# Kernel tuning notes

Measured on AMD Instinct MI355X. Metric: run time of the kernel, lower is better.

The kernel has to match this reference:

```python
import jax, jax.numpy as jnp
import numpy as np


def setup_inputs() -> dict:
    key = jax.random.key(0)
    ks = jax.random.split(key, 9)
    B, S, E, H, D = 8, 1000, 1024, 16, 64
    sc = 0.02
    return {
        "x": jax.random.normal(ks[0], (B, S, E), dtype=jnp.float32),
        "wq": jax.random.normal(ks[1], (H, E, D), dtype=jnp.float32) * sc,
        "bq": jax.random.normal(ks[2], (H, D), dtype=jnp.float32) * sc,
        "wk": jax.random.normal(ks[3], (H, E, D), dtype=jnp.float32) * sc,
        "bk": jax.random.normal(ks[4], (H, D), dtype=jnp.float32) * sc,
        "wv": jax.random.normal(ks[5], (H, E, D), dtype=jnp.float32) * sc,
        "bv": jax.random.normal(ks[6], (H, D), dtype=jnp.float32) * sc,
        "wp": jax.random.normal(ks[7], (E, E), dtype=jnp.float32) * sc,
        "bp": jax.random.normal(ks[8], (E,), dtype=jnp.float32) * sc,
    }


def reference(x, wq, bq, wk, bk, wv, bv, wp, bp):
    B, S, E = x.shape
    H, _, D = wq.shape
    # per-head projections, all heads batched: [B,H,S,D]
    q = jnp.einsum('bse,hed->bhsd', x, wq) + bq[None, :, None, :]
    k = jnp.einsum('bse,hed->bhsd', x, wk) + bk[None, :, None, :]
    v = jnp.einsum('bse,hed->bhsd', x, wv) + bv[None, :, None, :]
    # NOTE: original scales by sqrt(seq_len), not sqrt(head_dim)
    scores = jnp.einsum('bhsd,bhtd->bhst', q, k) / jnp.asarray(S, x.dtype) ** 0.5
    causal = jnp.tril(jnp.ones((S, S), dtype=bool))  # mask[:S,:S] == 1 keeps
    scores = jnp.where(causal, scores, jnp.asarray(-jnp.inf, x.dtype))
    attn = jax.nn.softmax(scores, axis=-1)
    z = jnp.einsum('bhst,bhtd->bhsd', attn, v)
    # concat heads in head order -> [B,S,E]
    y = z.transpose(0, 2, 1, 3).reshape(B, S, E)
    # projection then exact GELU (dropout is identity at eval)
    return jax.nn.gelu(jnp.einsum('bse,ef->bsf', y, wp) + bp, approximate=False)
```

## Files before the change

### kernel.cpp

```cpp
#include <hip/hip_runtime.h>
#include <hip/hip_bf16.h>
#include <math.h>

constexpr int B_ = 8, S_ = 1000, E_ = 1024, H_ = 16, D_ = 64;
constexpr int M_ = B_ * S_;

using bf16x8 = __attribute__((ext_vector_type(8))) __bf16;
using u16x8  = __attribute__((ext_vector_type(8))) unsigned short;
using f32x4  = __attribute__((ext_vector_type(4))) float;

static __device__ __forceinline__ unsigned short f2bf(float f) {
    union { float f; unsigned u; } c; c.f = f;
    return (unsigned short)((c.u + 0x7FFF + ((c.u >> 16) & 1)) >> 16);
}
static __device__ __forceinline__ unsigned short f2bf_fast(float f) {
    union { float f; unsigned u; } c; c.f = f;
    return (unsigned short)((c.u + 0x8000) >> 16);
}
static __device__ __forceinline__ float bfr2f(unsigned short s) {
    union { unsigned u; float f; } c; c.u = ((unsigned)s) << 16;
    return c.f;
}

__global__ __launch_bounds__(256) void cast_x_kernel(
    const float* __restrict__ x, unsigned short* __restrict__ xbf)
{
    const size_t i = ((size_t)blockIdx.x * 256 + threadIdx.x) * 4;
    float4 v = *(const float4*)(x + i);
    ushort4 o;
    o.x = f2bf(v.x); o.y = f2bf(v.y); o.z = f2bf(v.z); o.w = f2bf(v.w);
    *(ushort4*)(xbf + i) = o;
}

__global__ __launch_bounds__(256) void transpose_wqkv_kernel(
    const float* __restrict__ wq, const float* __restrict__ wk,
    const float* __restrict__ wv, unsigned short* __restrict__ WT)
{
    __shared__ unsigned short Ts[64 * 65];
    const int et = blockIdx.x, zh = blockIdx.y;
    const int z = zh >> 4, h = zh & 15;
    const float* src = (z == 0 ? wq : z == 1 ? wk : wv) + (size_t)h * E_ * D_;

    const int d = threadIdx.x & 63;
    const int e0 = threadIdx.x >> 6;
    #pragma unroll
    for (int p = 0; p < 16; ++p) {
        const int e = e0 + p * 4;
        Ts[d * 65 + e] = f2bf(src[(size_t)(et * 64 + e) * D_ + d]);
    }
    __syncthreads();
    const int e = threadIdx.x & 63;
    const int d0 = threadIdx.x >> 6;
    #pragma unroll
    for (int p = 0; p < 16; ++p) {
        const int dd = d0 + p * 4;
        WT[((size_t)zh * 64 + dd) * E_ + et * 64 + e] = Ts[dd * 65 + e];
    }
}

__global__ __launch_bounds__(256) void transpose_wp_kernel(
    const float* __restrict__ wp, unsigned short* __restrict__ wpT)
{
    __shared__ unsigned short Ts[64 * 65];
    const int et = blockIdx.x, ft = blockIdx.y;
    const int f = threadIdx.x & 63;
    const int e0 = threadIdx.x >> 6;
    #pragma unroll
    for (int p = 0; p < 16; ++p) {
        const int e = e0 + p * 4;
        Ts[f * 65 + e] = f2bf(wp[(size_t)(et * 64 + e) * E_ + ft * 64 + f]);
    }
    __syncthreads();
    const int e = threadIdx.x & 63;
    const int f0 = threadIdx.x >> 6;
    #pragma unroll
    for (int p = 0; p < 16; ++p) {
        const int ff = f0 + p * 4;
        wpT[((size_t)(ft * 64 + ff)) * E_ + et * 64 + e] = Ts[ff * 65 + e];
    }
}

__global__ __launch_bounds__(256) void transpose_v_kernel(
    const unsigned short* __restrict__ vb, unsigned short* __restrict__ vt)
{
    __shared__ unsigned short Ts[64 * 65];
    const int st = blockIdx.x, bh = blockIdx.y;
    const size_t ibase = (size_t)bh * S_ * D_;
    const size_t obase = (size_t)bh * D_ * S_;

    const int d = threadIdx.x & 63;
    const int s0 = threadIdx.x >> 6;
    #pragma unroll
    for (int p = 0; p < 16; ++p) {
        const int s = s0 + p * 4;
        const int srow = st * 64 + s;
        Ts[s * 65 + d] = (srow < S_) ? vb[ibase + (size_t)srow * D_ + d] : 0;
    }
    __syncthreads();
    const int s = threadIdx.x & 63;
    const int d0 = threadIdx.x >> 6;
    const int scol = st * 64 + s;
    if (scol < S_) {
        #pragma unroll
        for (int p = 0; p < 16; ++p) {
            const int dd = d0 + p * 4;
            vt[obase + (size_t)dd * S_ + scol] = Ts[s * 65 + dd];
        }
    }
}

__global__ __launch_bounds__(256) void qkv_mfma_kernel(
    const unsigned short* __restrict__ xbf, const unsigned short* __restrict__ WT,
    const float* __restrict__ bq, const float* __restrict__ bk,
    const float* __restrict__ bv,
    unsigned short* __restrict__ qb, unsigned short* __restrict__ kb,
    unsigned short* __restrict__ vb)
{
    constexpr int P = 72;
    __shared__ unsigned short As[128 * P];
    __shared__ unsigned short Bs[3][64 * P];

    const int tid = threadIdx.x;
    const int wave = tid >> 6, lane = tid & 63;
    const int m16 = lane & 15, quad = lane >> 4;
    const int m0 = blockIdx.x * 128;
    const int h  = blockIdx.y;

    f32x4 acc[3][4][2];
    #pragma unroll
    for (int z = 0; z < 3; ++z)
        #pragma unroll
        for (int nt = 0; nt < 4; ++nt)
            #pragma unroll
            for (int mh = 0; mh < 2; ++mh)
                acc[z][nt][mh] = (f32x4){0.f, 0.f, 0.f, 0.f};

    const int ar = tid & 31;
    const int ac8 = (tid >> 5) * 8;
    const int bd = tid & 63;
    const int bc8 = (tid >> 6) * 8;

    for (int kk = 0; kk < E_; kk += 64) {
        __syncthreads();
        #pragma unroll
        for (int p = 0; p < 4; ++p) {
            const int r = ar + p * 32;
            int srow = m0 + r; if (srow >= M_) srow = M_ - 1;
            *(u16x8*)&As[r * P + ac8] =
                *(const u16x8*)(xbf + (size_t)srow * E_ + kk + ac8);
        }
        #pragma unroll
        for (int z = 0; z < 3; ++z) {
            const unsigned short* wb = WT + ((size_t)(z * 16 + h) * 64 + bd) * E_ + kk;
            *(u16x8*)&Bs[z][bd * P + bc8]      = *(const u16x8*)(wb + bc8);
            *(u16x8*)&Bs[z][bd * P + bc8 + 32] = *(const u16x8*)(wb + bc8 + 32);
        }
        __syncthreads();

        #pragma unroll
        for (int kh = 0; kh < 2; ++kh) {
            const int ko = kh * 32 + quad * 8;
            const bf16x8 a0 = *(const bf16x8*)&As[(wave * 32 + m16) * P + ko];
            const bf16x8 a1 = *(const bf16x8*)&As[(wave * 32 + 16 + m16) * P + ko];
            #pragma unroll
            for (int z = 0; z < 3; ++z)
                #pragma unroll
                for (int nt = 0; nt < 4; ++nt) {
                    const bf16x8 bfr = *(const bf16x8*)&Bs[z][(nt * 16 + m16) * P + ko];
                    acc[z][nt][0] = __builtin_amdgcn_mfma_f32_16x16x32_bf16(a0, bfr, acc[z][nt][0], 0, 0, 0);
                    acc[z][nt][1] = __builtin_amdgcn_mfma_f32_16x16x32_bf16(a1, bfr, acc[z][nt][1], 0, 0, 0);
                }
        }
    }

    float biasv[3][4];
    #pragma unroll
    for (int nt = 0; nt < 4; ++nt) {
        biasv[0][nt] = bq[h * D_ + nt * 16 + m16];
        biasv[1][nt] = bk[h * D_ + nt * 16 + m16];
        biasv[2][nt] = bv[h * D_ + nt * 16 + m16];
    }

    #pragma unroll
    for (int mh = 0; mh < 2; ++mh)
        #pragma unroll
        for (int r = 0; r < 4; ++r) {
            const int row = m0 + wave * 32 + mh * 16 + quad * 4 + r;
            if (row < M_) {
                const int b = row / S_, s = row % S_;
                const size_t ob = (((size_t)b * H_ + h) * S_ + s) * D_ + m16;
                #pragma unroll
                for (int nt = 0; nt < 4; ++nt) {
                    qb[ob + nt * 16] = f2bf(acc[0][nt][mh][r] + biasv[0][nt]);
                    kb[ob + nt * 16] = f2bf(acc[1][nt][mh][r] + biasv[1][nt]);
                    vb[ob + nt * 16] = f2bf(acc[2][nt][mh][r] + biasv[2][nt]);
                }
            }
        }
}

__global__ __launch_bounds__(256) void attn_flash_kernel(
    const unsigned short* __restrict__ q, const unsigned short* __restrict__ k,
    const unsigned short* __restrict__ vt, unsigned short* __restrict__ ybf)
{
    constexpr int P_ = 72;
    __shared__ unsigned short Qs[64 * P_];
    __shared__ unsigned short Ks[64 * P_];
    __shared__ unsigned short Vt[64 * P_];
    __shared__ unsigned short Ps[4][16 * P_];

    const int tid  = threadIdx.x;
    const int wave = tid >> 6, lane = tid & 63;
    const int m16  = lane & 15, quad = lane >> 4;
    const int qt = (int)gridDim.x - 1 - (int)blockIdx.x;
    const int h = blockIdx.y, b = blockIdx.z;
    const size_t bh  = ((size_t)b * H_ + h) * S_;
    const size_t vtb = ((size_t)b * H_ + h) * (size_t)D_ * S_;
    const float sl2e = 0.031622776601683794f * 1.4426950408889634f;

    const int c8 = (tid & 7) * 8;
    const int r0 = tid >> 3;

    #pragma unroll
    for (int rr = 0; rr < 64; rr += 32) {
        const int r = r0 + rr;
        const int srow = qt * 64 + r;
        u16x8 val = {0, 0, 0, 0, 0, 0, 0, 0};
        if (srow < S_) val = *(const u16x8*)(q + (bh + srow) * D_ + c8);
        u16x8 o;
        #pragma unroll
        for (int j = 0; j < 8; ++j) o[j] = f2bf_fast(bfr2f(val[j]) * sl2e);
        *(u16x8*)&Qs[r * P_ + c8] = o;
    }
    __syncthreads();

    const bf16x8 qa0 = *(const bf16x8*)&Qs[(wave * 16 + m16) * P_ + quad * 8];
    const bf16x8 qa1 = *(const bf16x8*)&Qs[(wave * 16 + m16) * P_ + 32 + quad * 8];

    f32x4 O[4] = {{0,0,0,0},{0,0,0,0},{0,0,0,0},{0,0,0,0}};
    float l_i[4] = {0.f, 0.f, 0.f, 0.f};

    const int qrow_base = qt * 64 + wave * 16 + quad * 4;

    u16x8 kreg[2], vreg[2];
    #pragma unroll
    for (int i = 0; i < 2; ++i) {
        const int srow = r0 + i * 32;
        kreg[i] = *(const u16x8*)(k + (bh + srow) * D_ + c8);
        vreg[i] = *(const u16x8*)(vt + vtb + (size_t)(r0 + i * 32) * S_ + c8);
    }

    for (int tt = 0; tt <= qt; ++tt) {
        const int t0 = tt * 64;
        __syncthreads();
        #pragma unroll
        for (int i = 0; i < 2; ++i) {
            *(u16x8*)&Ks[(r0 + i * 32) * P_ + c8] = kreg[i];
            *(u16x8*)&Vt[(r0 + i * 32) * P_ + c8] = vreg[i];
        }
        __syncthreads();

        if (tt < qt) {
            const int nt0 = t0 + 64;
            #pragma unroll
            for (int i = 0; i < 2; ++i) {
                const int t = r0 + i * 32;
                const int srow = nt0 + t;
                u16x8 kv = {0,0,0,0,0,0,0,0}, vv = {0,0,0,0,0,0,0,0};
                if (srow < S_) kv = *(const u16x8*)(k + (bh + srow) * D_ + c8);
                if (nt0 + c8 < S_)
                    vv = *(const u16x8*)(vt + vtb + (size_t)t * S_ + nt0 + c8);
                kreg[i] = kv; vreg[i] = vv;
            }
        }

        f32x4 sc[4];
        #pragma unroll
        for (int ts = 0; ts < 4; ++ts) {
            const bf16x8 kb0 = *(const bf16x8*)&Ks[(ts * 16 + m16) * P_ + quad * 8];
            const bf16x8 kb1 = *(const bf16x8*)&Ks[(ts * 16 + m16) * P_ + 32 + quad * 8];
            f32x4 a = {0.f, 0.f, 0.f, 0.f};
            a = __builtin_amdgcn_mfma_f32_16x16x32_bf16(qa0, kb0, a, 0, 0, 0);
            a = __builtin_amdgcn_mfma_f32_16x16x32_bf16(qa1, kb1, a, 0, 0, 0);
            sc[ts] = a;
        }

        unsigned short* const pw = &Ps[wave][0];
        if (tt == qt) {
            #pragma unroll
            for (int ts = 0; ts < 4; ++ts) {
                const int t = t0 + ts * 16 + m16;
                #pragma unroll
                for (int r = 0; r < 4; ++r) {
                    float p = __builtin_amdgcn_exp2f(sc[ts][r]);
                    p = (t <= qrow_base + r) ? p : 0.f;
                    pw[(quad * 4 + r) * P_ + ts * 16 + m16] = f2bf_fast(p);
                    l_i[r] += p;
                }
            }
        } else {
            #pragma unroll
            for (int ts = 0; ts < 4; ++ts)
                #pragma unroll
                for (int r = 0; r < 4; ++r) {
                    const float p = __builtin_amdgcn_exp2f(sc[ts][r]);
                    pw[(quad * 4 + r) * P_ + ts * 16 + m16] = f2bf_fast(p);
                    l_i[r] += p;
                }
        }

        const bf16x8 pa0 = *(const bf16x8*)&pw[m16 * P_ + quad * 8];
        const bf16x8 pa1 = *(const bf16x8*)&pw[m16 * P_ + 32 + quad * 8];
        #pragma unroll
        for (int db = 0; db < 4; ++db) {
            const bf16x8 vb0 = *(const bf16x8*)&Vt[(db * 16 + m16) * P_ + quad * 8];
            const bf16x8 vb1 = *(const bf16x8*)&Vt[(db * 16 + m16) * P_ + 32 + quad * 8];
            O[db] = __builtin_amdgcn_mfma_f32_16x16x32_bf16(pa0, vb0, O[db], 0, 0, 0);
            O[db] = __builtin_amdgcn_mfma_f32_16x16x32_bf16(pa1, vb1, O[db], 0, 0, 0);
        }
    }

    #pragma unroll
    for (int off = 1; off < 16; off <<= 1)
        #pragma unroll
        for (int r = 0; r < 4; ++r)
            l_i[r] += __shfl_xor(l_i[r], off, 64);

    #pragma unroll
    for (int r = 0; r < 4; ++r) {
        const int qrow = qrow_base + r;
        if (qrow < S_) {
            const float invl = 1.0f / l_i[r];
            #pragma unroll
            for (int db = 0; db < 4; ++db)
                ybf[((size_t)b * S_ + qrow) * E_ + h * D_ + db * 16 + m16] =
                    f2bf(O[db][r] * invl);
        }
    }
}

__global__ __launch_bounds__(256) void proj_mfma_kernel(
    const unsigned short* __restrict__ ybf, const unsigned short* __restrict__ wpT,
    const float* __restrict__ bp, float* __restrict__ out)
{
    constexpr int P = 72;
    __shared__ unsigned short As[128 * P];
    __shared__ unsigned short Bs[64 * P];

    const int tid = threadIdx.x;
    const int wave = tid >> 6, lane = tid & 63;
    const int m16 = lane & 15, quad = lane >> 4;
    const int m0 = blockIdx.x * 128;
    const int n0 = blockIdx.y * 64;

    f32x4 acc[4][2];
    #pragma unroll
    for (int nt = 0; nt < 4; ++nt)
        #pragma unroll
        for (int mh = 0; mh < 2; ++mh)
            acc[nt][mh] = (f32x4){0.f, 0.f, 0.f, 0.f};

    const int ar = tid & 31;
    const int ac8 = (tid >> 5) * 8;
    const int bd = tid & 63;
    const int bc8 = (tid >> 6) * 8;

    for (int kk = 0; kk < E_; kk += 64) {
        __syncthreads();
        #pragma unroll
        for (int p = 0; p < 4; ++p) {
            const int r = ar + p * 32;
            int srow = m0 + r; if (srow >= M_) srow = M_ - 1;
            *(u16x8*)&As[r * P + ac8] =
                *(const u16x8*)(ybf + (size_t)srow * E_ + kk + ac8);
        }
        {
            const unsigned short* wb = wpT + (size_t)(n0 + bd) * E_ + kk;
            *(u16x8*)&Bs[bd * P + bc8]      = *(const u16x8*)(wb + bc8);
            *(u16x8*)&Bs[bd * P + bc8 + 32] = *(const u16x8*)(wb + bc8 + 32);
        }
        __syncthreads();

        #pragma unroll
        for (int kh = 0; kh < 2; ++kh) {
            const int ko = kh * 32 + quad * 8;
            const bf16x8 a0 = *(const bf16x8*)&As[(wave * 32 + m16) * P + ko];
            const bf16x8 a1 = *(const bf16x8*)&As[(wave * 32 + 16 + m16) * P + ko];
            #pragma unroll
            for (int nt = 0; nt < 4; ++nt) {
                const bf16x8 bfr = *(const bf16x8*)&Bs[(nt * 16 + m16) * P + ko];
                acc[nt][0] = __builtin_amdgcn_mfma_f32_16x16x32_bf16(a0, bfr, acc[nt][0], 0, 0, 0);
                acc[nt][1] = __builtin_amdgcn_mfma_f32_16x16x32_bf16(a1, bfr, acc[nt][1], 0, 0, 0);
            }
        }
    }

    float biasv[4];
    #pragma unroll
    for (int nt = 0; nt < 4; ++nt) biasv[nt] = bp[n0 + nt * 16 + m16];

    #pragma unroll
    for (int mh = 0; mh < 2; ++mh)
        #pragma unroll
        for (int r = 0; r < 4; ++r) {
            const int row = m0 + wave * 32 + mh * 16 + quad * 4 + r;
            if (row < M_) {
                #pragma unroll
                for (int nt = 0; nt < 4; ++nt) {
                    const float t = acc[nt][mh][r] + biasv[nt];
                    const float g = 0.5f * t * (1.0f + erff(t * 0.70710678118654752f));
                    out[(size_t)row * E_ + n0 + nt * 16 + m16] = g;
                }
            }
        }
}

extern "C" void kernel_launch(void* const* d_in, const int* in_sizes, int n_in,
                              void* d_out, int out_size, void* d_ws, size_t ws_size,
                              hipStream_t stream)
{
    const float* x  = (const float*)d_in[0];
    const float* wq = (const float*)d_in[1];
    const float* bq = (const float*)d_in[2];
    const float* wk = (const float*)d_in[3];
    const float* bk = (const float*)d_in[4];
    const float* wv = (const float*)d_in[5];
    const float* bv = (const float*)d_in[6];
    const float* wp = (const float*)d_in[7];
    const float* bp = (const float*)d_in[8];
    float* out = (float*)d_out;

    const size_t nME = (size_t)M_ * E_;
    unsigned short* xbf = (unsigned short*)d_ws;
    unsigned short* WT  = xbf + nME;
    unsigned short* wpT = WT + 3145728;
    unsigned short* qb  = wpT + 1048576;
    unsigned short* kb  = qb + nME;
    unsigned short* vb  = kb + nME;
    unsigned short* ybf = vb + nME;
    unsigned short* vtr = ybf + nME;

    cast_x_kernel<<<dim3((unsigned)(nME / 1024)), 256, 0, stream>>>(x, xbf);
    transpose_wqkv_kernel<<<dim3(16, 48), 256, 0, stream>>>(wq, wk, wv, WT);
    transpose_wp_kernel<<<dim3(16, 16), 256, 0, stream>>>(wp, wpT);

    qkv_mfma_kernel<<<dim3((M_ + 127) / 128, H_), 256, 0, stream>>>(
        xbf, WT, bq, bk, bv, qb, kb, vb);
    transpose_v_kernel<<<dim3(16, B_ * H_), 256, 0, stream>>>(vb, vtr);
    attn_flash_kernel<<<dim3((S_ + 63) / 64, H_, B_), 256, 0, stream>>>(
        qb, kb, vtr, ybf);
    proj_mfma_kernel<<<dim3((M_ + 127) / 128, E_ / 64), 256, 0, stream>>>(
        ybf, wpT, bp, out);
}
```

Measured before the change: 329.2 us.

## Use 2x2 wave tiling and register prefetch in QKV and projection GEMMs

Both GEMM kernels now split the block tile across waves in a 2x2 layout (64 rows by 96 or 64 columns per wave) instead of each wave covering 32 rows by all columns. This raises MFMA work per LDS fragment load. Global loads for the next K tile are issued into registers right after the barrier, so they overlap with the MFMA work. The projection block tile grows from 128x64 to 128x128, halving its grid, while register pressure rises (24 and 16 accumulators per wave).

```diff
diff --git a/kernel.cpp b/kernel.cpp
--- a/kernel.cpp
+++ b/kernel.cpp
@@ -118,85 +118,115 @@
 {
     constexpr int P = 72;
     __shared__ unsigned short As[128 * P];
-    __shared__ unsigned short Bs[3][64 * P];
+    __shared__ unsigned short Bs[3 * 64 * P];
 
     const int tid = threadIdx.x;
     const int wave = tid >> 6, lane = tid & 63;
     const int m16 = lane & 15, quad = lane >> 4;
+    const int wm = wave >> 1, wn = wave & 1;
     const int m0 = blockIdx.x * 128;
     const int h  = blockIdx.y;
 
-    f32x4 acc[3][4][2];
-    #pragma unroll
-    for (int z = 0; z < 3; ++z)
-        #pragma unroll
-        for (int nt = 0; nt < 4; ++nt)
-            #pragma unroll
-            for (int mh = 0; mh < 2; ++mh)
-                acc[z][nt][mh] = (f32x4){0.f, 0.f, 0.f, 0.f};
+    f32x4 acc[6][4];
+    #pragma unroll
+    for (int nf = 0; nf < 6; ++nf)
+        #pragma unroll
+        for (int mf = 0; mf < 4; ++mf)
+            acc[nf][mf] = (f32x4){0.f, 0.f, 0.f, 0.f};
+
+    int boff[6];
+    #pragma unroll
+    for (int nf = 0; nf < 6; ++nf) {
+        const int cc = wn * 96 + nf * 16;
+        boff[6 - 1 - (5 - nf)] = (cc >> 6) * 64 * P + (cc & 63) * P;
+    }
 
     const int ar = tid & 31;
     const int ac8 = (tid >> 5) * 8;
     const int bd = tid & 63;
     const int bc8 = (tid >> 6) * 8;
 
+    int asrow[4];
+    #pragma unroll
+    for (int p = 0; p < 4; ++p) {
+        int r = m0 + ar + p * 32;
+        asrow[p] = (r < M_) ? r : (M_ - 1);
+    }
+
+    u16x8 areg[4], breg[3][2];
+    #pragma unroll
+    for (int p = 0; p < 4; ++p)
+        areg[p] = *(const u16x8*)(xbf + (size_t)asrow[p] * E_ + ac8);
+    #pragma unroll
+    for (int z = 0; z < 3; ++z) {
+        const unsigned short* wb = WT + ((size_t)(z * 16 + h) * 64 + bd) * E_;
+        breg[z][0] = *(const u16x8*)(wb + bc8);
+        breg[z][1] = *(const u16x8*)(wb + bc8 + 32);
+    }
+
     for (int kk = 0; kk < E_; kk += 64) {
         __syncthreads();
         #pragma unroll
-        for (int p = 0; p < 4; ++p) {
-            const int r = ar + p * 32;
-            int srow = m0 + r; if (srow >= M_) srow = M_ - 1;
-            *(u16x8*)&As[r * P + ac8] =
-                *(const u16x8*)(xbf + (size_t)srow * E_ + kk + ac8);
-        }
+        for (int p = 0; p < 4; ++p)
+            *(u16x8*)&As[(ar + p * 32) * P + ac8] = areg[p];
         #pragma unroll
         for (int z = 0; z < 3; ++z) {
-            const unsigned short* wb = WT + ((size_t)(z * 16 + h) * 64 + bd) * E_ + kk;
-            *(u16x8*)&Bs[z][bd * P + bc8]      = *(const u16x8*)(wb + bc8);
-            *(u16x8*)&Bs[z][bd * P + bc8 + 32] = *(const u16x8*)(wb + bc8 + 32);
+            *(u16x8*)&Bs[z * 64 * P + bd * P + bc8]      = breg[z][0];
+            *(u16x8*)&Bs[z * 64 * P + bd * P + bc8 + 32] = breg[z][1];
         }
         __syncthreads();
+
+        if (kk + 64 < E_) {
+            const int kn = kk + 64;
+            #pragma unroll
+            for (int p = 0; p < 4; ++p)
+                areg[p] = *(const u16x8*)(xbf + (size_t)asrow[p] * E_ + kn + ac8);
+            #pragma unroll
+            for (int z = 0; z < 3; ++z) {
+                const unsigned short* wb = WT + ((size_t)(z * 16 + h) * 64 + bd) * E_ + kn;
+                breg[z][0] = *(const u16x8*)(wb + bc8);
+                breg[z][1] = *(const u16x8*)(wb + bc8 + 32);
+            }
+        }
 
         #pragma unroll
         for (int kh = 0; kh < 2; ++kh) {
             const int ko = kh * 32 + quad * 8;
-            const bf16x8 a0 = *(const bf16x8*)&As[(wave * 32 + m16) * P + ko];
-            const bf16x8 a1 = *(const bf16x8*)&As[(wave * 32 + 16 + m16) * P + ko];
-            #pragma unroll
-            for (int z = 0; z < 3; ++z)
+            bf16x8 af[4];
+            #pragma unroll
+            for (int mf = 0; mf < 4; ++mf)
+                af[mf] = *(const bf16x8*)&As[(wm * 64 + mf * 16 + m16) * P + ko];
+            #pragma unroll
+            for (int nf = 0; nf < 6; ++nf) {
+                const bf16x8 bfr = *(const bf16x8*)&Bs[boff[nf] + m16 * P + ko];
                 #pragma unroll
-                for (int nt = 0; nt < 4; ++nt) {
-                    const bf16x8 bfr = *(const bf16x8*)&Bs[z][(nt * 16 + m16) * P + ko];
-                    acc[z][nt][0] = __builtin_amdgcn_mfma_f32_16x16x32_bf16(a0, bfr, acc[z][nt][0], 0, 0, 0);
-                    acc[z][nt][1] = __builtin_amdgcn_mfma_f32_16x16x32_bf16(a1, bfr, acc[z][nt][1], 0, 0, 0);
+                for (int mf = 0; mf < 4; ++mf)
+                    acc[nf][mf] = __builtin_amdgcn_mfma_f32_16x16x32_bf16(
+                        af[mf], bfr, acc[nf][mf], 0, 0, 0);
+            }
+        }
+    }
+
+    #pragma unroll
+    for (int nf = 0; nf < 6; ++nf) {
+        const int cc = wn * 96 + nf * 16;
+        const int zz = cc >> 6;
+        const int dd = (cc & 63) + m16;
+        unsigned short* const op = (zz == 0) ? qb : (zz == 1) ? kb : vb;
+        const float* const bp_  = (zz == 0) ? bq : (zz == 1) ? bk : bv;
+        const float biasv = bp_[h * D_ + dd];
+        #pragma unroll
+        for (int mf = 0; mf < 4; ++mf)
+            #pragma unroll
+            for (int r = 0; r < 4; ++r) {
+                const int row = m0 + wm * 64 + mf * 16 + quad * 4 + r;
+                if (row < M_) {
+                    const int b = row / S_, s = row % S_;
+                    op[(((size_t)b * H_ + h) * S_ + s) * D_ + dd] =
+                        f2bf(acc[nf][mf][r] + biasv);
                 }
-        }
-    }
-
-    float biasv[3][4];
-    #pragma unroll
-    for (int nt = 0; nt < 4; ++nt) {
-        biasv[0][nt] = bq[h * D_ + nt * 16 + m16];
-        biasv[1][nt] = bk[h * D_ + nt * 16 + m16];
-        biasv[2][nt] = bv[h * D_ + nt * 16 + m16];
-    }
-
-    #pragma unroll
-    for (int mh = 0; mh < 2; ++mh)
-        #pragma unroll
-        for (int r = 0; r < 4; ++r) {
-            const int row = m0 + wave * 32 + mh * 16 + quad * 4 + r;
-            if (row < M_) {
-                const int b = row / S_, s = row % S_;
-                const size_t ob = (((size_t)b * H_ + h) * S_ + s) * D_ + m16;
-                #pragma unroll
-                for (int nt = 0; nt < 4; ++nt) {
-                    qb[ob + nt * 16] = f2bf(acc[0][nt][mh][r] + biasv[0][nt]);
-                    kb[ob + nt * 16] = f2bf(acc[1][nt][mh][r] + biasv[1][nt]);
-                    vb[ob + nt * 16] = f2bf(acc[2][nt][mh][r] + biasv[2][nt]);
-                }
-            }
-        }
+            }
+    }
 }
 
 __global__ __launch_bounds__(256) void attn_flash_kernel(
@@ -345,71 +375,92 @@
 {
     constexpr int P = 72;
     __shared__ unsigned short As[128 * P];
-    __shared__ unsigned short Bs[64 * P];
+    __shared__ unsigned short Bs[128 * P];
 
     const int tid = threadIdx.x;
     const int wave = tid >> 6, lane = tid & 63;
     const int m16 = lane & 15, quad = lane >> 4;
+    const int wm = wave >> 1, wn = wave & 1;
     const int m0 = blockIdx.x * 128;
-    const int n0 = blockIdx.y * 64;
-
-    f32x4 acc[4][2];
-    #pragma unroll
-    for (int nt = 0; nt < 4; ++nt)
-        #pragma unroll
-        for (int mh = 0; mh < 2; ++mh)
-            acc[nt][mh] = (f32x4){0.f, 0.f, 0.f, 0.f};
+    const int n0 = blockIdx.y * 128;
+
+    f32x4 acc[4][4];
+    #pragma unroll
+    for (int nf = 0; nf < 4; ++nf)
+        #pragma unroll
+        for (int mf = 0; mf < 4; ++mf)
+            acc[nf][mf] = (f32x4){0.f, 0.f, 0.f, 0.f};
 
     const int ar = tid & 31;
     const int ac8 = (tid >> 5) * 8;
-    const int bd = tid & 63;
-    const int bc8 = (tid >> 6) * 8;
+
+    int asrow[4];
+    #pragma unroll
+    for (int p = 0; p < 4; ++p) {
+        int r = m0 + ar + p * 32;
+        asrow[p] = (r < M_) ? r : (M_ - 1);
+    }
+
+    u16x8 areg[4], breg[4];
+    #pragma unroll
+    for (int p = 0; p < 4; ++p) {
+        areg[p] = *(const u16x8*)(ybf + (size_t)asrow[p] * E_ + ac8);
+        breg[p] = *(const u16x8*)(wpT + (size_t)(n0 + ar + p * 32) * E_ + ac8);
+    }
 
     for (int kk = 0; kk < E_; kk += 64) {
         __syncthreads();
         #pragma unroll
         for (int p = 0; p < 4; ++p) {
-            const int r = ar + p * 32;
-            int srow = m0 + r; if (srow >= M_) srow = M_ - 1;
-            *(u16x8*)&As[r * P + ac8] =
-                *(const u16x8*)(ybf + (size_t)srow * E_ + kk + ac8);
-        }
-        {
-            const unsigned short* wb = wpT + (size_t)(n0 + bd) * E_ + kk;
-            *(u16x8*)&Bs[bd * P + bc8]      = *(const u16x8*)(wb + bc8);
-            *(u16x8*)&Bs[bd * P + bc8 + 32] = *(const u16x8*)(wb + bc8 + 32);
+            *(u16x8*)&As[(ar + p * 32) * P + ac8] = areg[p];
+            *(u16x8*)&Bs[(ar + p * 32) * P + ac8] = breg[p];
         }
         __syncthreads();
+
+        if (kk + 64 < E_) {
+            const int kn = kk + 64;
+            #pragma unroll
+            for (int p = 0; p < 4; ++p) {
+                areg[p] = *(const u16x8*)(ybf + (size_t)asrow[p] * E_ + kn + ac8);
+                breg[p] = *(const u16x8*)(wpT + (size_t)(n0 + ar + p * 32) * E_ + kn + ac8);
+            }
+        }
 
         #pragma unroll
         for (int kh = 0; kh < 2; ++kh) {
             const int ko = kh * 32 + quad * 8;
-            const bf16x8 a0 = *(const bf16x8*)&As[(wave * 32 + m16) * P + ko];
-            const bf16x8 a1 = *(const bf16x8*)&As[(wave * 32 + 16 + m16) * P + ko];
-            #pragma unroll
-            for (int nt = 0; nt < 4; ++nt) {
-                const bf16x8 bfr = *(const bf16x8*)&Bs[(nt * 16 + m16) * P + ko];
-                acc[nt][0] = __builtin_amdgcn_mfma_f32_16x16x32_bf16(a0, bfr, acc[nt][0], 0, 0, 0);
-                acc[nt][1] = __builtin_amdgcn_mfma_f32_16x16x32_bf16(a1, bfr, acc[nt][1], 0, 0, 0);
+            bf16x8 af[4];
+            #pragma unroll
+            for (int mf = 0; mf < 4; ++mf)
+                af[mf] = *(const bf16x8*)&As[(wm * 64 + mf * 16 + m16) * P + ko];
+            #pragma unroll
+            for (int nf = 0; nf < 4; ++nf) {
+                const bf16x8 bfr = *(const bf16x8*)&Bs[(wn * 64 + nf * 16 + m16) * P + ko];
+                #pragma unroll
+                for (int mf = 0; mf < 4; ++mf)
+                    acc[nf][mf] = __builtin_amdgcn_mfma_f32_16x16x32_bf16(
+                        af[mf], bfr, acc[nf][mf], 0, 0, 0);
             }
         }
     }
 
     float biasv[4];
     #pragma unroll
-    for (int nt = 0; nt < 4; ++nt) biasv[nt] = bp[n0 + nt * 16 + m16];
-
-    #pragma unroll
-    for (int mh = 0; mh < 2; ++mh)
+    for (int nf = 0; nf < 4; ++nf)
+        biasv[nf] = bp[n0 + wn * 64 + nf * 16 + m16];
+
+    #pragma unroll
+    for (int mf = 0; mf < 4; ++mf)
         #pragma unroll
         for (int r = 0; r < 4; ++r) {
-            const int row = m0 + wave * 32 + mh * 16 + quad * 4 + r;
+            const int row = m0 + wm * 64 + mf * 16 + quad * 4 + r;
             if (row < M_) {
                 #pragma unroll
-                for (int nt = 0; nt < 4; ++nt) {
-                    const float t = acc[nt][mh][r] + biasv[nt];
+                for (int nf = 0; nf < 4; ++nf) {
+                    const int col = n0 + wn * 64 + nf * 16 + m16;
+                    const float t = acc[nf][mf][r] + biasv[nf];
                     const float g = 0.5f * t * (1.0f + erff(t * 0.70710678118654752f));
-                    out[(size_t)row * E_ + n0 + nt * 16 + m16] = g;
+                    out[(size_t)row * E_ + col] = g;
                 }
             }
         }
@@ -449,6 +500,6 @@
     transpose_v_kernel<<<dim3(16, B_ * H_), 256, 0, stream>>>(vb, vtr);
     attn_flash_kernel<<<dim3((S_ + 63) / 64, H_, B_), 256, 0, stream>>>(
         qb, kb, vtr, ybf);
-    proj_mfma_kernel<<<dim3((M_ + 127) / 128, E_ / 64), 256, 0, stream>>>(
+    proj_mfma_kernel<<<dim3((M_ + 127) / 128, E_ / 128), 256, 0, stream>>>(
         ybf, wpT, bp, out);
 }
```

Measured after the change: 379.4 us. +15.2%, slower.

## Enlarge projection GEMM tile to 128x128 with register-prefetched global loads

Applied to the files above, without the earlier changes.

The output projection kernel now computes 128x128 tiles, with waves arranged 2x2 and each wave holding 64x64 of output, instead of 128x64 tiles. Each block loads the next K-slice of A and B into registers while the current slice is computed from LDS. This raises arithmetic intensity and halves redundant A-tile reads. The cost is higher register pressure (64 accumulator floats plus prefetch registers) and half as many blocks, which may lower occupancy.

```diff
diff --git a/kernel.cpp b/kernel.cpp
--- a/kernel.cpp
+++ b/kernel.cpp
@@ -345,71 +345,92 @@
 {
     constexpr int P = 72;
     __shared__ unsigned short As[128 * P];
-    __shared__ unsigned short Bs[64 * P];
+    __shared__ unsigned short Bs[128 * P];
 
     const int tid = threadIdx.x;
     const int wave = tid >> 6, lane = tid & 63;
     const int m16 = lane & 15, quad = lane >> 4;
+    const int wm = wave >> 1, wn = wave & 1;
     const int m0 = blockIdx.x * 128;
-    const int n0 = blockIdx.y * 64;
-
-    f32x4 acc[4][2];
-    #pragma unroll
-    for (int nt = 0; nt < 4; ++nt)
-        #pragma unroll
-        for (int mh = 0; mh < 2; ++mh)
-            acc[nt][mh] = (f32x4){0.f, 0.f, 0.f, 0.f};
+    const int n0 = blockIdx.y * 128;
+
+    f32x4 acc[4][4];
+    #pragma unroll
+    for (int nf = 0; nf < 4; ++nf)
+        #pragma unroll
+        for (int mf = 0; mf < 4; ++mf)
+            acc[nf][mf] = (f32x4){0.f, 0.f, 0.f, 0.f};
 
     const int ar = tid & 31;
     const int ac8 = (tid >> 5) * 8;
-    const int bd = tid & 63;
-    const int bc8 = (tid >> 6) * 8;
+
+    int asrow[4];
+    #pragma unroll
+    for (int p = 0; p < 4; ++p) {
+        int r = m0 + ar + p * 32;
+        asrow[p] = (r < M_) ? r : (M_ - 1);
+    }
+
+    u16x8 areg[4], breg[4];
+    #pragma unroll
+    for (int p = 0; p < 4; ++p) {
+        areg[p] = *(const u16x8*)(ybf + (size_t)asrow[p] * E_ + ac8);
+        breg[p] = *(const u16x8*)(wpT + (size_t)(n0 + ar + p * 32) * E_ + ac8);
+    }
 
     for (int kk = 0; kk < E_; kk += 64) {
         __syncthreads();
         #pragma unroll
         for (int p = 0; p < 4; ++p) {
-            const int r = ar + p * 32;
-            int srow = m0 + r; if (srow >= M_) srow = M_ - 1;
-            *(u16x8*)&As[r * P + ac8] =
-                *(const u16x8*)(ybf + (size_t)srow * E_ + kk + ac8);
-        }
-        {
-            const unsigned short* wb = wpT + (size_t)(n0 + bd) * E_ + kk;
-            *(u16x8*)&Bs[bd * P + bc8]      = *(const u16x8*)(wb + bc8);
-            *(u16x8*)&Bs[bd * P + bc8 + 32] = *(const u16x8*)(wb + bc8 + 32);
-        }
-        __syncthreads();
+            *(u16x8*)&As[(ar + p * 32) * P + ac8] = areg[p];
+            *(u16x8*)&Bs[(ar + p * 32) * P + ac8] = breg[p];
+        }
+        __syncthreads();
+
+        if (kk + 64 < E_) {
+            const int kn = kk + 64;
+            #pragma unroll
+            for (int p = 0; p < 4; ++p) {
+                areg[p] = *(const u16x8*)(ybf + (size_t)asrow[p] * E_ + kn + ac8);
+                breg[p] = *(const u16x8*)(wpT + (size_t)(n0 + ar + p * 32) * E_ + kn + ac8);
+            }
+        }
 
         #pragma unroll
         for (int kh = 0; kh < 2; ++kh) {
             const int ko = kh * 32 + quad * 8;
-            const bf16x8 a0 = *(const bf16x8*)&As[(wave * 32 + m16) * P + ko];
-            const bf16x8 a1 = *(const bf16x8*)&As[(wave * 32 + 16 + m16) * P + ko];
-            #pragma unroll
-            for (int nt = 0; nt < 4; ++nt) {
-                const bf16x8 bfr = *(const bf16x8*)&Bs[(nt * 16 + m16) * P + ko];
-                acc[nt][0] = __builtin_amdgcn_mfma_f32_16x16x32_bf16(a0, bfr, acc[nt][0], 0, 0, 0);
-                acc[nt][1] = __builtin_amdgcn_mfma_f32_16x16x32_bf16(a1, bfr, acc[nt][1], 0, 0, 0);
+            bf16x8 af[4];
+            #pragma unroll
+            for (int mf = 0; mf < 4; ++mf)
+                af[mf] = *(const bf16x8*)&As[(wm * 64 + mf * 16 + m16) * P + ko];
+            #pragma unroll
+            for (int nf = 0; nf < 4; ++nf) {
+                const bf16x8 bfr = *(const bf16x8*)&Bs[(wn * 64 + nf * 16 + m16) * P + ko];
+                #pragma unroll
+                for (int mf = 0; mf < 4; ++mf)
+                    acc[nf][mf] = __builtin_amdgcn_mfma_f32_16x16x32_bf16(
+                        af[mf], bfr, acc[nf][mf], 0, 0, 0);
             }
         }
     }
 
     float biasv[4];
     #pragma unroll
-    for (int nt = 0; nt < 4; ++nt) biasv[nt] = bp[n0 + nt * 16 + m16];
-
-    #pragma unroll
-    for (int mh = 0; mh < 2; ++mh)
+    for (int nf = 0; nf < 4; ++nf)
+        biasv[nf] = bp[n0 + wn * 64 + nf * 16 + m16];
+
+    #pragma unroll
+    for (int mf = 0; mf < 4; ++mf)
         #pragma unroll
         for (int r = 0; r < 4; ++r) {
-            const int row = m0 + wave * 32 + mh * 16 + quad * 4 + r;
+            const int row = m0 + wm * 64 + mf * 16 + quad * 4 + r;
             if (row < M_) {
                 #pragma unroll
-                for (int nt = 0; nt < 4; ++nt) {
-                    const float t = acc[nt][mh][r] + biasv[nt];
+                for (int nf = 0; nf < 4; ++nf) {
+                    const int col = n0 + wn * 64 + nf * 16 + m16;
+                    const float t = acc[nf][mf][r] + biasv[nf];
                     const float g = 0.5f * t * (1.0f + erff(t * 0.70710678118654752f));
-                    out[(size_t)row * E_ + n0 + nt * 16 + m16] = g;
+                    out[(size_t)row * E_ + col] = g;
                 }
             }
         }
@@ -449,6 +470,6 @@
     transpose_v_kernel<<<dim3(16, B_ * H_), 256, 0, stream>>>(vb, vtr);
     attn_flash_kernel<<<dim3((S_ + 63) / 64, H_, B_), 256, 0, stream>>>(
         qb, kb, vtr, ybf);
-    proj_mfma_kernel<<<dim3((M_ + 127) / 128, E_ / 64), 256, 0, stream>>>(
+    proj_mfma_kernel<<<dim3((M_ + 127) / 128, E_ / 128), 256, 0, stream>>>(
         ybf, wpT, bp, out);
 }
```

Result: faster. 309.7 us (-5.9%).
